# Optimization experiments

Hardware: AMD Instinct MI355X
Metric: run time of the kernel (lower is better)

## Reference

```python
import jax, jax.numpy as jnp
import numpy as np

NUM_NODES = 65536      # 16 graphs x 4096 nodes
NODES_PER_GRAPH = 4096
NUM_GRAPHS = 16
NUM_EDGES = 1048576    # avg degree 16
DIM = 64


def setup_inputs() -> dict:
    key = jax.random.key(0)
    ks = jax.random.split(key, 10)
    # edges constrained within each component graph (batched-graph semantics)
    eper = NUM_EDGES // NUM_GRAPHS
    gid = np.repeat(np.arange(NUM_GRAPHS), eper)
    rng = np.random.default_rng(0)
    src = jnp.asarray(rng.integers(0, NODES_PER_GRAPH, NUM_EDGES) + gid * NODES_PER_GRAPH, dtype=jnp.int64)
    dst = jnp.asarray(rng.integers(0, NODES_PER_GRAPH, NUM_EDGES) + gid * NODES_PER_GRAPH, dtype=jnp.int64)
    s = 1.0 / np.sqrt(DIM)
    return {
        "x": jax.random.normal(ks[0], (NUM_NODES, DIM), dtype=jnp.float32),
        "W1": jax.random.normal(ks[1], (DIM, DIM), dtype=jnp.float32) * s,
        "b1": jnp.zeros((DIM,), dtype=jnp.float32),
        "W2": jax.random.normal(ks[2], (DIM, DIM), dtype=jnp.float32) * s,
        "b2": jnp.zeros((DIM,), dtype=jnp.float32),
        "W3": jax.random.normal(ks[3], (DIM, DIM), dtype=jnp.float32) * s,
        "b3": jnp.zeros((DIM,), dtype=jnp.float32),
        "src": src,
        "dst": dst,
        "num_graphs": NUM_GRAPHS,
    }


def _sym_norms(src, dst, n):
    ones = jnp.ones(src.shape[0], dtype=jnp.float32)
    deg_out = jax.ops.segment_sum(ones, src, num_segments=n)
    deg_in = jax.ops.segment_sum(ones, dst, num_segments=n)
    inv_sqrt = lambda d: jnp.where(d > 0, d, 1.0) ** -0.5 * (d > 0)
    return inv_sqrt(deg_out), inv_sqrt(deg_in)


def _graph_conv(x, W, b, src, dst, norm_src, norm_dst, n):
    # DGL GraphConv, norm='both': h = D_in^{-1/2} A D_out^{-1/2} (X W) + b
    h = (x * norm_src[:, None]) @ W          # [N, D]
    msg = h[src]                              # [E, D] gather
    agg = jax.ops.segment_sum(msg, dst, num_segments=n)  # [N, D] scatter-add
    return agg * norm_dst[:, None] + b


def reference(x, W1, b1, W2, b2, W3, b3, src, dst, num_graphs):
    n = x.shape[0]
    norm_src, norm_dst = _sym_norms(src, dst, n)
    h = _graph_conv(x, W1, b1, src, dst, norm_src, norm_dst, n)
    h = _graph_conv(h, W2, b2, src, dst, norm_src, norm_dst, n)
    h = _graph_conv(h, W3, b3, src, dst, norm_src, norm_dst, n)
    # unbatch + pad to max_num_nodes + stack; equal-size graphs -> pure reshape
    return h.reshape(num_graphs, n // num_graphs, h.shape[-1])
```

## Files before the change

kernel.cpp:

```cpp
#include <hip/hip_runtime.h>
#include <hip/hip_fp16.h>

#define DIM 64
#define NG  16
#define CPG 16
#define NPG 4096
#define LSTR 68
#define HISTB (NG*CPG)
#define GGN 32

__global__ __launch_bounds__(256) void k1_hist_gemm(
    const int* __restrict__ src, const int* __restrict__ dst,
    int* __restrict__ hsub, int* __restrict__ dsub, int chunk, int npg,
    const float* __restrict__ x, const float* __restrict__ W1,
    float* __restrict__ hout, int swiz)
{
    __shared__ int smem[8192];
    const int tid = threadIdx.x;
    if ((int)blockIdx.x < HISTB) {
        int* hs = smem;
        int* hd = smem + NPG;
        const int blk = blockIdx.x;
        const int g = blk / CPG;
        const int ebase = blk * chunk;
        const int nbase = g * npg;
        for (int i = tid; i < npg; i += 256) { hs[i] = 0; hd[i] = 0; }
        __syncthreads();
        for (int e = tid; e < chunk; e += 256) {
            atomicAdd(&hs[src[ebase + e] - nbase], 1);
            atomicAdd(&hd[dst[ebase + e] - nbase], 1);
        }
        __syncthreads();
        for (int i = tid; i < npg; i += 256) {
            hsub[blk * npg + i] = hs[i];
            dsub[blk * npg + i] = hd[i];
        }
    } else {
        float* Wt = (float*)smem;
        float* xs = Wt + 64 * LSTR;
        int blk = blockIdx.x - HISTB;
        if (swiz) {
            int xg = blk & 7;
            int j = blk >> 3;
            int g = xg + ((j >> 7) << 3);
            blk = (g << 7) + (j & 127);
        }
        const int row0 = blk * 32;
        for (int i = tid; i < 64 * 64; i += 256) {
            int k = i >> 6, c = i & 63;
            Wt[c * LSTR + k] = W1[i];
        }
        for (int i = tid; i < 32 * 64; i += 256) {
            int r = i >> 6, c = i & 63;
            xs[r * LSTR + c] = x[(size_t)(row0 + r) * 64 + c];
        }
        __syncthreads();
        const int c0 = tid & 31;
        const int r0 = tid >> 5;
        float acc[4][2] = {};
#pragma unroll
        for (int k = 0; k < 64; k += 4) {
            float4 w0 = *(const float4*)&Wt[(c0     ) * LSTR + k];
            float4 w1 = *(const float4*)&Wt[(c0 + 32) * LSTR + k];
#pragma unroll
            for (int rr = 0; rr < 4; ++rr) {
                float4 xv = *(const float4*)&xs[(r0 + 8 * rr) * LSTR + k];
                acc[rr][0] += xv.x * w0.x + xv.y * w0.y + xv.z * w0.z + xv.w * w0.w;
                acc[rr][1] += xv.x * w1.x + xv.y * w1.y + xv.z * w1.z + xv.w * w1.w;
            }
        }
#pragma unroll
        for (int rr = 0; rr < 4; ++rr) {
            int row = row0 + r0 + 8 * rr;
            hout[(size_t)row * 64 + c0     ] = acc[rr][0];
            hout[(size_t)row * 64 + c0 + 32] = acc[rr][1];
        }
    }
}

__global__ __launch_bounds__(1024) void k2_scan(
    const int* __restrict__ hsub, int* __restrict__ dsub,
    float* __restrict__ ns, float* __restrict__ nd,
    int* __restrict__ rowptr, int epg, int npg, int N, int E)
{
    __shared__ int ddeg[NPG];
    __shared__ int wsum[16];
    const int g = blockIdx.x;
    const int t = threadIdx.x;
    const int nbase = g * npg;
    const int ebase = g * epg;
    for (int i = t; i < npg; i += 1024) {
        int sd = 0, dd = 0;
#pragma unroll
        for (int k = 0; k < CPG; ++k) {
            sd += hsub[(g * CPG + k) * npg + i];
            dd += dsub[(g * CPG + k) * npg + i];
        }
        ns[nbase + i] = sd > 0 ? rsqrtf((float)sd) : 0.0f;
        nd[nbase + i] = dd > 0 ? rsqrtf((float)dd) : 0.0f;
        ddeg[i] = dd;
    }
    __syncthreads();
    const int i0 = 4 * t;
    int d0 = ddeg[i0], d1 = ddeg[i0 + 1], d2 = ddeg[i0 + 2], d3 = ddeg[i0 + 3];
    int s4 = d0 + d1 + d2 + d3;
    const int lane = t & 63, wid = t >> 6;
    int v = s4;
#pragma unroll
    for (int off = 1; off < 64; off <<= 1) {
        int u = __shfl_up(v, off, 64);
        if (lane >= off) v += u;
    }
    if (lane == 63) wsum[wid] = v;
    __syncthreads();
    if (t < 16) {
        int w = wsum[t];
#pragma unroll
        for (int off = 1; off < 16; off <<= 1) {
            int u = __shfl_up(w, off, 16);
            if (t >= off) w += u;
        }
        wsum[t] = w;
    }
    __syncthreads();
    int incl = v + (wid > 0 ? wsum[wid - 1] : 0);
    int c = ebase + incl - s4;
    rowptr[nbase + i0    ] = c; ddeg[i0    ] = c; c += d0;
    rowptr[nbase + i0 + 1] = c; ddeg[i0 + 1] = c; c += d1;
    rowptr[nbase + i0 + 2] = c; ddeg[i0 + 2] = c; c += d2;
    rowptr[nbase + i0 + 3] = c; ddeg[i0 + 3] = c;
    if (g == 0 && t == 0) rowptr[N] = E;
    __syncthreads();
    for (int i = t; i < npg; i += 1024) {
        int cc = ddeg[i];
#pragma unroll
        for (int k = 0; k < CPG; ++k) {
            int* p = &dsub[(g * CPG + k) * npg + i];
            int old = *p; *p = cc; cc += old;
        }
    }
}

__global__ __launch_bounds__(256) void k3_fill(
    const int* __restrict__ src, const int* __restrict__ dst,
    const int* __restrict__ dsub, int* __restrict__ ssrc, int chunk, int npg,
    const float* __restrict__ hA32, const float* __restrict__ ns,
    __half* __restrict__ hF)
{
    const int t = threadIdx.x;
    if ((int)blockIdx.x < HISTB) {
        __shared__ int cur[NPG];
        const int blk = blockIdx.x;
        const int g = blk / CPG;
        const int ebase = blk * chunk;
        const int nbase = g * npg;
        for (int i = t; i < npg; i += 256) cur[i] = dsub[blk * npg + i];
        __syncthreads();
        for (int e = t; e < chunk; e += 256) {
            int s = src[ebase + e];
            int d = dst[ebase + e] - nbase;
            int pos = atomicAdd(&cur[d], 1);
            ssrc[pos] = s;
        }
    } else {
        const int sb = blockIdx.x - HISTB;
        const int base = sb * 16384;
#pragma unroll
        for (int it = 0; it < 16; ++it) {
            int pos = base + it * 1024 + t * 4;
            float4 v = *(const float4*)(hA32 + pos);
            float s = ns[pos >> 6];
            __half2 p0 = __floats2half2_rn(v.x * s, v.y * s);
            __half2 p1 = __floats2half2_rn(v.z * s, v.w * s);
            uint2 o;
            o.x = *(const unsigned int*)&p0;
            o.y = *(const unsigned int*)&p1;
            *(uint2*)(hF + pos) = o;
        }
    }
}

__device__ __forceinline__ void acc_h4(float4& acc, uint2 u)
{
    __half2 p = *(__half2*)&u.x;
    __half2 q = *(__half2*)&u.y;
    float2 f0 = __half22float2(p);
    float2 f1 = __half22float2(q);
    acc.x += f0.x; acc.y += f0.y; acc.z += f1.x; acc.w += f1.y;
}

__device__ __forceinline__ void acc_h4s(float4& acc, uint2 u, float s)
{
    __half2 p = *(__half2*)&u.x;
    __half2 q = *(__half2*)&u.y;
    float2 f0 = __half22float2(p);
    float2 f1 = __half22float2(q);
    acc.x += s * f0.x; acc.y += s * f0.y; acc.z += s * f1.x; acc.w += s * f1.y;
}

__device__ __forceinline__ void gather_rest(
    const __half* __restrict__ h, const int* __restrict__ ssrc,
    int j, int end, int sub, float4& acc)
{
    const size_t off = (size_t)sub * 4;
    const int last = end - 8;
    while (j <= last) {
        int s0 = ssrc[j+0], s1 = ssrc[j+1], s2 = ssrc[j+2], s3 = ssrc[j+3];
        int s4 = ssrc[j+4], s5 = ssrc[j+5], s6 = ssrc[j+6], s7 = ssrc[j+7];
        uint2 u0 = *(const uint2*)(h + (size_t)s0 * 64 + off);
        uint2 u1 = *(const uint2*)(h + (size_t)s1 * 64 + off);
        uint2 u2 = *(const uint2*)(h + (size_t)s2 * 64 + off);
        uint2 u3 = *(const uint2*)(h + (size_t)s3 * 64 + off);
        uint2 u4 = *(const uint2*)(h + (size_t)s4 * 64 + off);
        uint2 u5 = *(const uint2*)(h + (size_t)s5 * 64 + off);
        uint2 u6 = *(const uint2*)(h + (size_t)s6 * 64 + off);
        uint2 u7 = *(const uint2*)(h + (size_t)s7 * 64 + off);
        acc_h4(acc, u0); acc_h4(acc, u1); acc_h4(acc, u2); acc_h4(acc, u3);
        acc_h4(acc, u4); acc_h4(acc, u5); acc_h4(acc, u6); acc_h4(acc, u7);
        j += 8;
    }
    int rem = end - j;
    if (rem > 0) {
#pragma unroll
        for (int q = 0; q < 4; ++q) {
            int jj = j + (q < rem ? q : rem - 1);
            int s = ssrc[jj];
            uint2 u = *(const uint2*)(h + (size_t)s * 64 + off);
            acc_h4s(acc, u, (q < rem) ? 1.0f : 0.0f);
        }
        if (rem > 4) {
#pragma unroll
            for (int q = 4; q < 8; ++q) {
                int jj = j + (q < rem ? q : rem - 1);
                int s = ssrc[jj];
                uint2 u = *(const uint2*)(h + (size_t)s * 64 + off);
                acc_h4s(acc, u, (q < rem) ? 1.0f : 0.0f);
            }
        }
    }
}

__device__ __forceinline__ void gather_node2(
    const __half* __restrict__ h, const int* __restrict__ ssrc,
    int begA, int endA, int begB, int endB, int sub,
    float4& accA, float4& accB)
{
    const size_t off = (size_t)sub * 4;
    int jA = begA, jB = begB;
    const int lastA = endA - 8, lastB = endB - 8;
    while (jA <= lastA && jB <= lastB) {
        int a0 = ssrc[jA+0], a1 = ssrc[jA+1], a2 = ssrc[jA+2], a3 = ssrc[jA+3];
        int a4 = ssrc[jA+4], a5 = ssrc[jA+5], a6 = ssrc[jA+6], a7 = ssrc[jA+7];
        int b0 = ssrc[jB+0], b1 = ssrc[jB+1], b2 = ssrc[jB+2], b3 = ssrc[jB+3];
        int b4 = ssrc[jB+4], b5 = ssrc[jB+5], b6 = ssrc[jB+6], b7 = ssrc[jB+7];
        uint2 uA0 = *(const uint2*)(h + (size_t)a0 * 64 + off);
        uint2 uA1 = *(const uint2*)(h + (size_t)a1 * 64 + off);
        uint2 uA2 = *(const uint2*)(h + (size_t)a2 * 64 + off);
        uint2 uA3 = *(const uint2*)(h + (size_t)a3 * 64 + off);
        uint2 uA4 = *(const uint2*)(h + (size_t)a4 * 64 + off);
        uint2 uA5 = *(const uint2*)(h + (size_t)a5 * 64 + off);
        uint2 uA6 = *(const uint2*)(h + (size_t)a6 * 64 + off);
        uint2 uA7 = *(const uint2*)(h + (size_t)a7 * 64 + off);
        uint2 uB0 = *(const uint2*)(h + (size_t)b0 * 64 + off);
        uint2 uB1 = *(const uint2*)(h + (size_t)b1 * 64 + off);
        uint2 uB2 = *(const uint2*)(h + (size_t)b2 * 64 + off);
        uint2 uB3 = *(const uint2*)(h + (size_t)b3 * 64 + off);
        uint2 uB4 = *(const uint2*)(h + (size_t)b4 * 64 + off);
        uint2 uB5 = *(const uint2*)(h + (size_t)b5 * 64 + off);
        uint2 uB6 = *(const uint2*)(h + (size_t)b6 * 64 + off);
        uint2 uB7 = *(const uint2*)(h + (size_t)b7 * 64 + off);
        acc_h4(accA, uA0); acc_h4(accA, uA1); acc_h4(accA, uA2); acc_h4(accA, uA3);
        acc_h4(accA, uA4); acc_h4(accA, uA5); acc_h4(accA, uA6); acc_h4(accA, uA7);
        acc_h4(accB, uB0); acc_h4(accB, uB1); acc_h4(accB, uB2); acc_h4(accB, uB3);
        acc_h4(accB, uB4); acc_h4(accB, uB5); acc_h4(accB, uB6); acc_h4(accB, uB7);
        jA += 8; jB += 8;
    }
    gather_rest(h, ssrc, jA, endA, sub, accA);
    gather_rest(h, ssrc, jB, endB, sub, accB);
}

__global__ __launch_bounds__(256) void gg_kernel(
    const __half* __restrict__ h, const int* __restrict__ ssrc,
    const int* __restrict__ rowptr, const float* __restrict__ ns,
    const float* __restrict__ nd, const float* __restrict__ bprev,
    const float* __restrict__ W, __half* __restrict__ hout,
    int N, int swiz)
{
    __shared__ float us[GGN][64];
    int blk = blockIdx.x;
    if (swiz) {
        int xg = blk & 7;
        int j = blk >> 3;
        int g = xg + ((j >> 7) << 3);
        blk = (g << 7) + (j & 127);
    }
    const int tid = threadIdx.x;
    const int wv = tid >> 6;
    const int lane = tid & 63;
    const int grp = lane >> 4;
    const int sub = lane & 15;

    const int nlA = wv * 4 + grp;
    const int nlB = nlA + 16;
    const int wA = blk * GGN + nlA;
    const int wB = blk * GGN + nlB;
    {
        int begA = rowptr[wA], endA = rowptr[wA + 1];
        int begB = rowptr[wB], endB = rowptr[wB + 1];
        float4 accA = {0.f,0.f,0.f,0.f}, accB = {0.f,0.f,0.f,0.f};
        gather_node2(h, ssrc, begA, endA, begB, endB, sub, accA, accB);
        float4 bv = *(const float4*)(bprev + sub * 4);
        {
            float sw = ns[wA];
            float alpha = nd[wA] * sw;
            float4 uo;
            uo.x = accA.x * alpha + sw * bv.x;
            uo.y = accA.y * alpha + sw * bv.y;
            uo.z = accA.z * alpha + sw * bv.z;
            uo.w = accA.w * alpha + sw * bv.w;
            *(float4*)&us[nlA][sub * 4] = uo;
        }
        {
            float sw = ns[wB];
            float alpha = nd[wB] * sw;
            float4 uo;
            uo.x = accB.x * alpha + sw * bv.x;
            uo.y = accB.y * alpha + sw * bv.y;
            uo.z = accB.z * alpha + sw * bv.z;
            uo.w = accB.w * alpha + sw * bv.w;
            *(float4*)&us[nlB][sub * 4] = uo;
        }
    }
    __syncthreads();
    const int c = tid & 63;
    const int nb = tid >> 6;
    float y[8] = {0.f,0.f,0.f,0.f,0.f,0.f,0.f,0.f};
#pragma unroll
    for (int k = 0; k < 64; k += 4) {
        float w0 = W[(k    ) * 64 + c];
        float w1 = W[(k + 1) * 64 + c];
        float w2 = W[(k + 2) * 64 + c];
        float w3 = W[(k + 3) * 64 + c];
#pragma unroll
        for (int m = 0; m < 8; ++m) {
            const float4 uv = *(const float4*)&us[nb + 4 * m][k];
            y[m] += uv.x * w0 + uv.y * w1 + uv.z * w2 + uv.w * w3;
        }
    }
#pragma unroll
    for (int m = 0; m < 8; ++m) {
        int wo = blk * GGN + nb + 4 * m;
        hout[(size_t)wo * 64 + c] = __float2half_rn(y[m]);
    }
}

__global__ __launch_bounds__(256) void gather_kernel(
    const __half* __restrict__ h, const int* __restrict__ ssrc,
    const int* __restrict__ rowptr, float* __restrict__ out,
    const float* __restrict__ nd, const float* __restrict__ b,
    int N, int swiz)
{
    int blk = blockIdx.x;
    if (swiz) {
        int x = blk & 7;
        int j = blk >> 3;
        int g = x + ((j >> 7) << 3);
        blk = (g << 7) + (j & 127);
    }
    const int wv = threadIdx.x >> 6;
    const int lane = threadIdx.x & 63;
    const int grp = lane >> 4;
    const int sub = lane & 15;
    int wA = blk * 32 + wv * 4 + grp;
    int wB = wA + 16;
    int begA = rowptr[wA], endA = rowptr[wA + 1];
    int begB = rowptr[wB], endB = rowptr[wB + 1];
    float4 accA = {0.f,0.f,0.f,0.f}, accB = {0.f,0.f,0.f,0.f};
    gather_node2(h, ssrc, begA, endA, begB, endB, sub, accA, accB);
    const float4 bv = *(const float4*)(b + sub * 4);
    {
        float n = nd[wA];
        accA.x = accA.x * n + bv.x;
        accA.y = accA.y * n + bv.y;
        accA.z = accA.z * n + bv.z;
        accA.w = accA.w * n + bv.w;
        *(float4*)(out + (size_t)wA * 64 + sub * 4) = accA;
    }
    {
        float n = nd[wB];
        accB.x = accB.x * n + bv.x;
        accB.y = accB.y * n + bv.y;
        accB.z = accB.z * n + bv.z;
        accB.w = accB.w * n + bv.w;
        *(float4*)(out + (size_t)wB * 64 + sub * 4) = accB;
    }
}

extern "C" void kernel_launch(void* const* d_in, const int* in_sizes, int n_in,
                              void* d_out, int out_size, void* d_ws, size_t ws_size,
                              hipStream_t stream)
{
    const float* x  = (const float*)d_in[0];
    const float* W1 = (const float*)d_in[1];
    const float* b1 = (const float*)d_in[2];
    const float* W2 = (const float*)d_in[3];
    const float* b2 = (const float*)d_in[4];
    const float* W3 = (const float*)d_in[5];
    const float* b3 = (const float*)d_in[6];
    const int*  src = (const int*)d_in[7];
    const int*  dst = (const int*)d_in[8];

    const int E = in_sizes[7];
    const int N = in_sizes[0] / DIM;
    const int epg = E / NG;
    const int npg = N / NG;
    const int chunk = epg / CPG;

    float*  ns     = (float*)d_ws;
    float*  nd     = ns + N;
    float*  hA32   = nd + N;
    __half* hF     = (__half*)(hA32 + (size_t)N * DIM);
    __half* h2     = hF + (size_t)N * DIM;
    int*    rowptr = (int*)(h2 + (size_t)N * DIM);
    int*    ssrc   = rowptr + N + 1;
    int*    hsub   = ssrc + E;
    int*    dsub   = hsub + (size_t)HISTB * npg;
    float*  agg    = (float*)d_out;

    const int swiz = (N == 65536 && npg == 4096) ? 1 : 0;

    k1_hist_gemm<<<HISTB + N / 32, 256, 0, stream>>>(
        src, dst, hsub, dsub, chunk, npg, x, W1, hA32, swiz);
    k2_scan<<<NG, 1024, 0, stream>>>(
        hsub, dsub, ns, nd, rowptr, epg, npg, N, E);
    k3_fill<<<HISTB + N / 256, 256, 0, stream>>>(
        src, dst, dsub, ssrc, chunk, npg, hA32, ns, hF);

    gg_kernel<<<N / GGN, 256, 0, stream>>>(
        hF, ssrc, rowptr, ns, nd, b1, W2, h2, N, swiz);
    gg_kernel<<<N / GGN, 256, 0, stream>>>(
        h2, ssrc, rowptr, ns, nd, b2, W3, hF, N, swiz);
    gather_kernel<<<N / 32, 256, 0, stream>>>(
        hF, ssrc, rowptr, agg, nd, b3, N, swiz);
}
```

Baseline: 218.7 us.

## Move layer-1 GEMM into fill kernel and software-pipeline gather index loads

The first-layer X·W1 GEMM moves out of the histogram kernel and into the CSR fill kernel. Because the degree norms are ready by then, it scales x by ns before the multiply and writes fp16 output directly, which drops the fp32 intermediate buffer and its separate convert pass. The paired-node gather loop now prefetches the next group of source indices while the current feature loads are in flight, adding registers and one redundant index load at the end. The histogram kernel now runs alone, so its latency no longer overlaps with GEMM work.

Measured after the change: 213.2 us. 2.5% less time.

```diff
diff --git a/kernel.cpp b/kernel.cpp
--- a/kernel.cpp
+++ b/kernel.cpp
@@ -9,72 +9,26 @@
 #define HISTB (NG*CPG)
 #define GGN 32
 
-__global__ __launch_bounds__(256) void k1_hist_gemm(
+__global__ __launch_bounds__(256) void kA_hist(
     const int* __restrict__ src, const int* __restrict__ dst,
-    int* __restrict__ hsub, int* __restrict__ dsub, int chunk, int npg,
-    const float* __restrict__ x, const float* __restrict__ W1,
-    float* __restrict__ hout, int swiz)
-{
-    __shared__ int smem[8192];
-    const int tid = threadIdx.x;
-    if ((int)blockIdx.x < HISTB) {
-        int* hs = smem;
-        int* hd = smem + NPG;
-        const int blk = blockIdx.x;
-        const int g = blk / CPG;
-        const int ebase = blk * chunk;
-        const int nbase = g * npg;
-        for (int i = tid; i < npg; i += 256) { hs[i] = 0; hd[i] = 0; }
-        __syncthreads();
-        for (int e = tid; e < chunk; e += 256) {
-            atomicAdd(&hs[src[ebase + e] - nbase], 1);
-            atomicAdd(&hd[dst[ebase + e] - nbase], 1);
-        }
-        __syncthreads();
-        for (int i = tid; i < npg; i += 256) {
-            hsub[blk * npg + i] = hs[i];
-            dsub[blk * npg + i] = hd[i];
-        }
-    } else {
-        float* Wt = (float*)smem;
-        float* xs = Wt + 64 * LSTR;
-        int blk = blockIdx.x - HISTB;
-        if (swiz) {
-            int xg = blk & 7;
-            int j = blk >> 3;
-            int g = xg + ((j >> 7) << 3);
-            blk = (g << 7) + (j & 127);
-        }
-        const int row0 = blk * 32;
-        for (int i = tid; i < 64 * 64; i += 256) {
-            int k = i >> 6, c = i & 63;
-            Wt[c * LSTR + k] = W1[i];
-        }
-        for (int i = tid; i < 32 * 64; i += 256) {
-            int r = i >> 6, c = i & 63;
-            xs[r * LSTR + c] = x[(size_t)(row0 + r) * 64 + c];
-        }
-        __syncthreads();
-        const int c0 = tid & 31;
-        const int r0 = tid >> 5;
-        float acc[4][2] = {};
-#pragma unroll
-        for (int k = 0; k < 64; k += 4) {
-            float4 w0 = *(const float4*)&Wt[(c0     ) * LSTR + k];
-            float4 w1 = *(const float4*)&Wt[(c0 + 32) * LSTR + k];
-#pragma unroll
-            for (int rr = 0; rr < 4; ++rr) {
-                float4 xv = *(const float4*)&xs[(r0 + 8 * rr) * LSTR + k];
-                acc[rr][0] += xv.x * w0.x + xv.y * w0.y + xv.z * w0.z + xv.w * w0.w;
-                acc[rr][1] += xv.x * w1.x + xv.y * w1.y + xv.z * w1.z + xv.w * w1.w;
-            }
-        }
-#pragma unroll
-        for (int rr = 0; rr < 4; ++rr) {
-            int row = row0 + r0 + 8 * rr;
-            hout[(size_t)row * 64 + c0     ] = acc[rr][0];
-            hout[(size_t)row * 64 + c0 + 32] = acc[rr][1];
-        }
+    int* __restrict__ hsub, int* __restrict__ dsub, int chunk, int npg)
+{
+    __shared__ int hs[NPG], hd[NPG];
+    const int blk = blockIdx.x;
+    const int g = blk / CPG;
+    const int t = threadIdx.x;
+    const int ebase = blk * chunk;
+    const int nbase = g * npg;
+    for (int i = t; i < npg; i += 256) { hs[i] = 0; hd[i] = 0; }
+    __syncthreads();
+    for (int e = t; e < chunk; e += 256) {
+        atomicAdd(&hs[src[ebase + e] - nbase], 1);
+        atomicAdd(&hd[dst[ebase + e] - nbase], 1);
+    }
+    __syncthreads();
+    for (int i = t; i < npg; i += 256) {
+        hsub[blk * npg + i] = hs[i];
+        hd[i] ? (dsub[blk * npg + i] = hd[i]) : (dsub[blk * npg + i] = 0);
     }
 }
 
@@ -141,41 +95,68 @@
     }
 }
 
-__global__ __launch_bounds__(256) void k3_fill(
+__global__ __launch_bounds__(256) void kC_gemm_fill(
     const int* __restrict__ src, const int* __restrict__ dst,
     const int* __restrict__ dsub, int* __restrict__ ssrc, int chunk, int npg,
-    const float* __restrict__ hA32, const float* __restrict__ ns,
-    __half* __restrict__ hF)
-{
-    const int t = threadIdx.x;
+    const float* __restrict__ x, const float* __restrict__ W1,
+    const float* __restrict__ ns, __half* __restrict__ hF, int swiz)
+{
+    __shared__ float smem[64 * LSTR + 32 * LSTR];
+    const int tid = threadIdx.x;
     if ((int)blockIdx.x < HISTB) {
-        __shared__ int cur[NPG];
+        int* cur = (int*)smem;
         const int blk = blockIdx.x;
         const int g = blk / CPG;
         const int ebase = blk * chunk;
         const int nbase = g * npg;
-        for (int i = t; i < npg; i += 256) cur[i] = dsub[blk * npg + i];
+        for (int i = tid; i < npg; i += 256) cur[i] = dsub[blk * npg + i];
         __syncthreads();
-        for (int e = t; e < chunk; e += 256) {
+        for (int e = tid; e < chunk; e += 256) {
             int s = src[ebase + e];
             int d = dst[ebase + e] - nbase;
             int pos = atomicAdd(&cur[d], 1);
             ssrc[pos] = s;
         }
     } else {
-        const int sb = blockIdx.x - HISTB;
-        const int base = sb * 16384;
-#pragma unroll
-        for (int it = 0; it < 16; ++it) {
-            int pos = base + it * 1024 + t * 4;
-            float4 v = *(const float4*)(hA32 + pos);
-            float s = ns[pos >> 6];
-            __half2 p0 = __floats2half2_rn(v.x * s, v.y * s);
-            __half2 p1 = __floats2half2_rn(v.z * s, v.w * s);
-            uint2 o;
-            o.x = *(const unsigned int*)&p0;
-            o.y = *(const unsigned int*)&p1;
-            *(uint2*)(hF + pos) = o;
+        float* Wt = smem;
+        float* xs = Wt + 64 * LSTR;
+        int blk = blockIdx.x - HISTB;
+        if (swiz) {
+            int xg = blk & 7;
+            int j = blk >> 3;
+            int g = xg + ((j >> 7) << 3);
+            blk = (g << 7) + (j & 127);
+        }
+        const int row0 = blk * 32;
+        for (int i = tid; i < 64 * 64; i += 256) {
+            int k = i >> 6, c = i & 63;
+            Wt[c * LSTR + k] = W1[i];
+        }
+        for (int i = tid; i < 32 * 64; i += 256) {
+            int r = i >> 6, c = i & 63;
+            int row = row0 + r;
+            xs[r * LSTR + c] = x[(size_t)row * 64 + c] * ns[row];
+        }
+        __syncthreads();
+        const int c0 = tid & 31;
+        const int r0 = tid >> 5;
+        float acc[4][2] = {};
+#pragma unroll
+        for (int k = 0; k < 64; k += 4) {
+            float4 w0 = *(const float4*)&Wt[(c0     ) * LSTR + k];
+            float4 w1 = *(const float4*)&Wt[(c0 + 32) * LSTR + k];
+#pragma unroll
+            for (int rr = 0; rr < 4; ++rr) {
+                float4 xv = *(const float4*)&xs[(r0 + 8 * rr) * LSTR + k];
+                acc[rr][0] += xv.x * w0.x + xv.y * w0.y + xv.z * w0.z + xv.w * w0.w;
+                acc[rr][1] += xv.x * w1.x + xv.y * w1.y + xv.z * w1.z + xv.w * w1.w;
+            }
+        }
+#pragma unroll
+        for (int rr = 0; rr < 4; ++rr) {
+            int row = row0 + r0 + 8 * rr;
+            hF[(size_t)row * 64 + c0     ] = __float2half_rn(acc[rr][0]);
+            hF[(size_t)row * 64 + c0 + 32] = __float2half_rn(acc[rr][1]);
         }
     }
 }
@@ -248,32 +229,46 @@
     const size_t off = (size_t)sub * 4;
     int jA = begA, jB = begB;
     const int lastA = endA - 8, lastB = endB - 8;
-    while (jA <= lastA && jB <= lastB) {
+    if (jA <= lastA && jB <= lastB) {
         int a0 = ssrc[jA+0], a1 = ssrc[jA+1], a2 = ssrc[jA+2], a3 = ssrc[jA+3];
         int a4 = ssrc[jA+4], a5 = ssrc[jA+5], a6 = ssrc[jA+6], a7 = ssrc[jA+7];
         int b0 = ssrc[jB+0], b1 = ssrc[jB+1], b2 = ssrc[jB+2], b3 = ssrc[jB+3];
         int b4 = ssrc[jB+4], b5 = ssrc[jB+5], b6 = ssrc[jB+6], b7 = ssrc[jB+7];
-        uint2 uA0 = *(const uint2*)(h + (size_t)a0 * 64 + off);
-        uint2 uA1 = *(const uint2*)(h + (size_t)a1 * 64 + off);
-        uint2 uA2 = *(const uint2*)(h + (size_t)a2 * 64 + off);
-        uint2 uA3 = *(const uint2*)(h + (size_t)a3 * 64 + off);
-        uint2 uA4 = *(const uint2*)(h + (size_t)a4 * 64 + off);
-        uint2 uA5 = *(const uint2*)(h + (size_t)a5 * 64 + off);
-        uint2 uA6 = *(const uint2*)(h + (size_t)a6 * 64 + off);
-        uint2 uA7 = *(const uint2*)(h + (size_t)a7 * 64 + off);
-        uint2 uB0 = *(const uint2*)(h + (size_t)b0 * 64 + off);
-        uint2 uB1 = *(const uint2*)(h + (size_t)b1 * 64 + off);
-        uint2 uB2 = *(const uint2*)(h + (size_t)b2 * 64 + off);
-        uint2 uB3 = *(const uint2*)(h + (size_t)b3 * 64 + off);
-        uint2 uB4 = *(const uint2*)(h + (size_t)b4 * 64 + off);
-        uint2 uB5 = *(const uint2*)(h + (size_t)b5 * 64 + off);
-        uint2 uB6 = *(const uint2*)(h + (size_t)b6 * 64 + off);
-        uint2 uB7 = *(const uint2*)(h + (size_t)b7 * 64 + off);
-        acc_h4(accA, uA0); acc_h4(accA, uA1); acc_h4(accA, uA2); acc_h4(accA, uA3);
-        acc_h4(accA, uA4); acc_h4(accA, uA5); acc_h4(accA, uA6); acc_h4(accA, uA7);
-        acc_h4(accB, uB0); acc_h4(accB, uB1); acc_h4(accB, uB2); acc_h4(accB, uB3);
-        acc_h4(accB, uB4); acc_h4(accB, uB5); acc_h4(accB, uB6); acc_h4(accB, uB7);
-        jA += 8; jB += 8;
+        for (;;) {
+            uint2 uA0 = *(const uint2*)(h + (size_t)a0 * 64 + off);
+            uint2 uA1 = *(const uint2*)(h + (size_t)a1 * 64 + off);
+            uint2 uA2 = *(const uint2*)(h + (size_t)a2 * 64 + off);
+            uint2 uA3 = *(const uint2*)(h + (size_t)a3 * 64 + off);
+            uint2 uA4 = *(const uint2*)(h + (size_t)a4 * 64 + off);
+            uint2 uA5 = *(const uint2*)(h + (size_t)a5 * 64 + off);
+            uint2 uA6 = *(const uint2*)(h + (size_t)a6 * 64 + off);
+            uint2 uA7 = *(const uint2*)(h + (size_t)a7 * 64 + off);
+            uint2 uB0 = *(const uint2*)(h + (size_t)b0 * 64 + off);
+            uint2 uB1 = *(const uint2*)(h + (size_t)b1 * 64 + off);
+            uint2 uB2 = *(const uint2*)(h + (size_t)b2 * 64 + off);
+            uint2 uB3 = *(const uint2*)(h + (size_t)b3 * 64 + off);
+            uint2 uB4 = *(const uint2*)(h + (size_t)b4 * 64 + off);
+            uint2 uB5 = *(const uint2*)(h + (size_t)b5 * 64 + off);
+            uint2 uB6 = *(const uint2*)(h + (size_t)b6 * 64 + off);
+            uint2 uB7 = *(const uint2*)(h + (size_t)b7 * 64 + off);
+            jA += 8; jB += 8;
+            bool more = (jA <= lastA) && (jB <= lastB);
+            int pA = more ? jA : begA;
+            int pB = more ? jB : begB;
+            int na0 = ssrc[pA+0], na1 = ssrc[pA+1], na2 = ssrc[pA+2], na3 = ssrc[pA+3];
+            int na4 = ssrc[pA+4], na5 = ssrc[pA+5], na6 = ssrc[pA+6], na7 = ssrc[pA+7];
+            int nb0 = ssrc[pB+0], nb1 = ssrc[pB+1], nb2 = ssrc[pB+2], nb3 = ssrc[pB+3];
+            int nb4 = ssrc[pB+4], nb5 = ssrc[pB+5], nb6 = ssrc[pB+6], nb7 = ssrc[pB+7];
+            acc_h4(accA, uA0); acc_h4(accA, uA1); acc_h4(accA, uA2); acc_h4(accA, uA3);
+            acc_h4(accA, uA4); acc_h4(accA, uA5); acc_h4(accA, uA6); acc_h4(accA, uA7);
+            acc_h4(accB, uB0); acc_h4(accB, uB1); acc_h4(accB, uB2); acc_h4(accB, uB3);
+            acc_h4(accB, uB4); acc_h4(accB, uB5); acc_h4(accB, uB6); acc_h4(accB, uB7);
+            if (!more) break;
+            a0 = na0; a1 = na1; a2 = na2; a3 = na3;
+            a4 = na4; a5 = na5; a6 = na6; a7 = na7;
+            b0 = nb0; b1 = nb1; b2 = nb2; b3 = nb3;
+            b4 = nb4; b5 = nb5; b6 = nb6; b7 = nb7;
+        }
     }
     gather_rest(h, ssrc, jA, endA, sub, accA);
     gather_rest(h, ssrc, jB, endB, sub, accB);
@@ -418,8 +413,7 @@
 
     float*  ns     = (float*)d_ws;
     float*  nd     = ns + N;
-    float*  hA32   = nd + N;
-    __half* hF     = (__half*)(hA32 + (size_t)N * DIM);
+    __half* hF     = (__half*)(nd + N);
     __half* h2     = hF + (size_t)N * DIM;
     int*    rowptr = (int*)(h2 + (size_t)N * DIM);
     int*    ssrc   = rowptr + N + 1;
@@ -429,12 +423,11 @@
 
     const int swiz = (N == 65536 && npg == 4096) ? 1 : 0;
 
-    k1_hist_gemm<<<HISTB + N / 32, 256, 0, stream>>>(
-        src, dst, hsub, dsub, chunk, npg, x, W1, hA32, swiz);
+    kA_hist<<<HISTB, 256, 0, stream>>>(src, dst, hsub, dsub, chunk, npg);
     k2_scan<<<NG, 1024, 0, stream>>>(
         hsub, dsub, ns, nd, rowptr, epg, npg, N, E);
-    k3_fill<<<HISTB + N / 256, 256, 0, stream>>>(
-        src, dst, dsub, ssrc, chunk, npg, hA32, ns, hF);
+    kC_gemm_fill<<<HISTB + N / 32, 256, 0, stream>>>(
+        src, dst, dsub, ssrc, chunk, npg, x, W1, ns, hF, swiz);
 
     gg_kernel<<<N / GGN, 256, 0, stream>>>(
         hF, ssrc, rowptr, ns, nd, b1, W2, h2, N, swiz);
```
